# Optimization experiments

Measured on AMD Instinct MI355X. Metric: run time of the kernel, lower is better.

Reference implementation:

```python
import jax, jax.numpy as jnp
import numpy as np

B = 131072
D = 64
H1 = 512
H2 = 256
NC = 128  # nurse classes
DC = 128  # doctor classes
EPS = 1e-5
NEG = -1e9


def _kaiming(key, fan_in, fan_out):
    # kaiming_normal_ with mode='fan_out', relu gain: std = sqrt(2/fan_out)
    return jax.random.normal(key, (fan_in, fan_out), jnp.float32) * jnp.sqrt(2.0 / fan_out)


def setup_inputs() -> dict:
    key = jax.random.key(0)
    ks = jax.random.split(key, 16)
    x = jax.random.normal(ks[0], (B, D), jnp.float32)
    sn = jax.random.randint(ks[1], (B,), 0, NC)
    sd = jax.random.randint(ks[2], (B,), 0, DC)
    # last-4 / last-3 columns carry the per-sample max class thresholds
    x = x.at[:, -4].set(sn.astype(jnp.float32)).at[:, -3].set(sd.astype(jnp.float32))
    inp = {
        'x': x,
        'W0': _kaiming(ks[3], D, H1), 'b0': jnp.zeros((H1,), jnp.float32),
        'g0': jnp.ones((H1,), jnp.float32), 'be0': jnp.zeros((H1,), jnp.float32),
        'rm0': jax.random.normal(ks[4], (H1,), jnp.float32) * 0.1,
        'rv0': jax.random.uniform(ks[5], (H1,), jnp.float32, 0.5, 1.5),
        'W1': _kaiming(ks[6], H1, H2), 'b1': jnp.zeros((H2,), jnp.float32),
        'g1': jnp.ones((H2,), jnp.float32), 'be1': jnp.zeros((H2,), jnp.float32),
        'rm1': jax.random.normal(ks[7], (H2,), jnp.float32) * 0.1,
        'rv1': jax.random.uniform(ks[8], (H2,), jnp.float32, 0.5, 1.5),
        'nW1': _kaiming(ks[9], H2, 64), 'nb1': jnp.zeros((64,), jnp.float32),
        'nW2': _kaiming(ks[10], 64, NC), 'nb2': jnp.zeros((NC,), jnp.float32),
        'dW1': _kaiming(ks[11], H2, 64), 'db1': jnp.zeros((64,), jnp.float32),
        'dW2': _kaiming(ks[12], 64, DC), 'db2': jnp.zeros((DC,), jnp.float32),
    }
    return inp


def _bn(h, g, be, rm, rv):
    # BatchNorm1d inference: normalize with running stats
    return (h - rm) * (g * jax.lax.rsqrt(rv + EPS)) + be


def reference(x, W0, b0, g0, be0, rm0, rv0, W1, b1, g1, be1, rm1, rv1,
              nW1, nb1, nW2, nb2, dW1, db1, dW2, db2):
    s_nurse = x[:, -4].astype(jnp.int32)   # [B]
    s_doctor = x[:, -3].astype(jnp.int32)  # [B]

    h = jax.nn.relu(_bn(x @ W0 + b0, g0, be0, rm0, rv0))   # [B,H1]
    h = jax.nn.relu(_bn(h @ W1 + b1, g1, be1, rm1, rv1))   # [B,H2]

    nurse_logits = jax.nn.relu(h @ nW1 + nb1) @ nW2 + nb2   # [B,NC]
    doctor_logits = jax.nn.relu(h @ dW1 + db1) @ dW2 + db2  # [B,DC]

    # vectorized range mask: positions <= s_max are kept
    nmask = (jnp.arange(NC)[None, :] <= s_nurse[:, None]).astype(nurse_logits.dtype)
    dmask = (jnp.arange(DC)[None, :] <= s_doctor[:, None]).astype(doctor_logits.dtype)
    nurse_logits = nurse_logits * nmask + (1.0 - nmask) * NEG
    doctor_logits = doctor_logits * dmask + (1.0 - dmask) * NEG
    return (nurse_logits, doctor_logits)
```

## Files before the change

### kernel.cpp

```cpp
#include <hip/hip_runtime.h>

#define NB 131072
#define NEG9 -1e9f

typedef __attribute__((ext_vector_type(8))) __bf16 bf16x8;
typedef __attribute__((ext_vector_type(4))) float f32x4;
typedef __attribute__((ext_vector_type(2))) unsigned int u32x2;
typedef __attribute__((ext_vector_type(4))) unsigned int u32x4;

__device__ __forceinline__ f32x4 mfma16(bf16x8 a, bf16x8 b, f32x4 c) {
    return __builtin_amdgcn_mfma_f32_16x16x32_bf16(a, b, c, 0, 0, 0);
}

__device__ __forceinline__ unsigned pk(float h, float l) {
    return __builtin_amdgcn_perm(__builtin_bit_cast(unsigned, h),
                                 __builtin_bit_cast(unsigned, l), 0x07060302u);
}
__device__ __forceinline__ unsigned pku(unsigned h, unsigned l) {
    return __builtin_amdgcn_perm(h, l, 0x07060302u);
}

__device__ __forceinline__ unsigned short f2bf(float f) {
    unsigned u = __builtin_bit_cast(unsigned, f);
    u += 0x7fffu + ((u >> 16) & 1u);
    return (unsigned short)(u >> 16);
}

struct __align__(16) Wspace {
    unsigned short W0t[512][64];
    unsigned short W1t[256][512];
    unsigned short nW1t[64][256];
    unsigned short dW1t[64][256];
    unsigned short nW2t[128][64];
    unsigned short dW2t[128][64];
    float c0[512];
    float c1[256];
    float nb1c[64], db1c[64];
    float nb2c[128], db2c[128];
};

__device__ Wspace g_ws;

__global__ void prep_kernel(
    const float* __restrict__ W0, const float* __restrict__ b0,
    const float* __restrict__ g0, const float* __restrict__ be0,
    const float* __restrict__ rm0, const float* __restrict__ rv0,
    const float* __restrict__ W1, const float* __restrict__ b1,
    const float* __restrict__ g1, const float* __restrict__ be1,
    const float* __restrict__ rm1, const float* __restrict__ rv1,
    const float* __restrict__ nW1, const float* __restrict__ nb1,
    const float* __restrict__ nW2, const float* __restrict__ nb2,
    const float* __restrict__ dW1, const float* __restrict__ db1,
    const float* __restrict__ dW2, const float* __restrict__ db2)
{
    const int tid = blockIdx.x * 256 + threadIdx.x;

    {
        int n = tid >> 9, k = tid & 511;
        float s = g1[n] * rsqrtf(rv1[n] + 1e-5f);
        ((unsigned short*)g_ws.W1t)[tid] = f2bf(W1[k * 256 + n] * s);
    }
    if (tid < 512 * 64) {
        int n = tid >> 6, k = tid & 63;
        float s = g0[n] * rsqrtf(rv0[n] + 1e-5f);
        ((unsigned short*)g_ws.W0t)[tid] = f2bf(W0[k * 512 + n] * s);
    }
    if (tid < 64 * 256) {
        int n = tid >> 8, k = tid & 255;
        ((unsigned short*)g_ws.nW1t)[tid] = f2bf(nW1[k * 64 + n]);
        ((unsigned short*)g_ws.dW1t)[tid] = f2bf(dW1[k * 64 + n]);
    }
    if (tid < 128 * 64) {
        int n = tid >> 6, k = tid & 63;
        ((unsigned short*)g_ws.nW2t)[tid] = f2bf(nW2[k * 128 + n]);
        ((unsigned short*)g_ws.dW2t)[tid] = f2bf(dW2[k * 128 + n]);
    }
    if (tid < 512) g_ws.c0[tid] = (b0[tid] - rm0[tid]) * (g0[tid] * rsqrtf(rv0[tid] + 1e-5f)) + be0[tid];
    if (tid < 256) g_ws.c1[tid] = (b1[tid] - rm1[tid]) * (g1[tid] * rsqrtf(rv1[tid] + 1e-5f)) + be1[tid];
    if (tid < 64) { g_ws.nb1c[tid] = nb1[tid]; g_ws.db1c[tid] = db1[tid]; }
    if (tid < 128) { g_ws.nb2c[tid] = nb2[tid]; g_ws.db2c[tid] = db2[tid]; }
}

__global__ __launch_bounds__(512, 4) void fused_mlp(
    const u32x4* __restrict__ xu, float* __restrict__ out)
{
    __shared__ __align__(16) unsigned short sXs [8 * 64 * 8];
    __shared__ __align__(16) unsigned short sReg[32 * 64 * 8];

    const int tid = threadIdx.x;
    const int w = tid >> 6;
    const int lane = tid & 63;
    const int m = lane & 15;
    const int q = lane >> 4;
    const int qh = q >> 1;
    const int ql = (q & 1) * 4;
    const int row0 = blockIdx.x * 64;

    {
        int r = tid >> 3, g = tid & 7;
        u32x4 v0 = __builtin_nontemporal_load(&xu[(size_t)(row0 + r) * 16 + g * 2]);
        u32x4 v1 = __builtin_nontemporal_load(&xu[(size_t)(row0 + r) * 16 + g * 2 + 1]);
        u32x4 p = { pku(v0[1], v0[0]), pku(v0[3], v0[2]), pku(v1[1], v1[0]), pku(v1[3], v1[2]) };
        *(u32x4*)&sXs[(g * 64 + r) * 8] = p;
    }
    __syncthreads();

    f32x4 acc1[2][4];
#pragma unroll
    for (int a = 0; a < 2; ++a)
#pragma unroll
        for (int b = 0; b < 4; ++b) acc1[a][b] = f32x4{0.f, 0.f, 0.f, 0.f};

    for (int ch = 0; ch < 2; ++ch) {
#pragma unroll
        for (int nt = 0; nt < 2; ++nt) {
            const int gcb = ch * 256 + w * 32 + nt * 16;
            bf16x8 wa0 = *(const bf16x8*)&g_ws.W0t[gcb + m][q * 8];
            bf16x8 wa1 = *(const bf16x8*)&g_ws.W0t[gcb + m][32 + q * 8];
            f32x4 bias = *(const f32x4*)&g_ws.c0[gcb + q * 4];
            const int kg = w * 4 + nt * 2 + qh;
#pragma unroll
            for (int mt = 0; mt < 4; ++mt) {
                bf16x8 xq0 = *(const bf16x8*)&sXs[(q * 64 + mt * 16 + m) * 8];
                bf16x8 xq1 = *(const bf16x8*)&sXs[((4 + q) * 64 + mt * 16 + m) * 8];
                f32x4 c = {0.f, 0.f, 0.f, 0.f};
                c = mfma16(wa0, xq0, c);
                c = mfma16(wa1, xq1, c);
                u32x2 pw = { pk(fmaxf(c[1] + bias[1], 0.f), fmaxf(c[0] + bias[0], 0.f)),
                             pk(fmaxf(c[3] + bias[3], 0.f), fmaxf(c[2] + bias[2], 0.f)) };
                *(u32x2*)&sReg[(kg * 64 + mt * 16 + m) * 8 + ql] = pw;
            }
        }
        __syncthreads();

#pragma unroll
        for (int ks = 0; ks < 8; ++ks) {
            bf16x8 wb[2], ab[4];
#pragma unroll
            for (int nt = 0; nt < 2; ++nt)
                wb[nt] = *(const bf16x8*)&g_ws.W1t[w * 32 + nt * 16 + m][ch * 256 + ks * 32 + q * 8];
#pragma unroll
            for (int mt = 0; mt < 4; ++mt)
                ab[mt] = *(const bf16x8*)&sReg[((ks * 4 + q) * 64 + mt * 16 + m) * 8];
#pragma unroll
            for (int nt = 0; nt < 2; ++nt)
#pragma unroll
                for (int mt = 0; mt < 4; ++mt)
                    acc1[nt][mt] = mfma16(wb[nt], ab[mt], acc1[nt][mt]);
        }
        __syncthreads();
    }

#pragma unroll
    for (int nt = 0; nt < 2; ++nt) {
        const int cb = w * 32 + nt * 16;
        f32x4 bias = *(const f32x4*)&g_ws.c1[cb + q * 4];
        const int kg = w * 4 + nt * 2 + qh;
#pragma unroll
        for (int mt = 0; mt < 4; ++mt) {
            f32x4 c = acc1[nt][mt];
            u32x2 pw = { pk(fmaxf(c[1] + bias[1], 0.f), fmaxf(c[0] + bias[0], 0.f)),
                         pk(fmaxf(c[3] + bias[3], 0.f), fmaxf(c[2] + bias[2], 0.f)) };
            *(u32x2*)&sReg[(kg * 64 + mt * 16 + m) * 8 + ql] = pw;
        }
    }
    __syncthreads();

    const int head = w >> 2;
    {
        const int cb = (w & 3) * 16;
        const unsigned short (*Wh)[256] = head ? g_ws.dW1t : g_ws.nW1t;
        const float* bh = head ? g_ws.db1c : g_ws.nb1c;
        f32x4 acc[4];
#pragma unroll
        for (int b = 0; b < 4; ++b) acc[b] = f32x4{0.f, 0.f, 0.f, 0.f};
#pragma unroll
        for (int ks = 0; ks < 8; ++ks) {
            bf16x8 wh = *(const bf16x8*)&Wh[cb + m][ks * 32 + q * 8];
#pragma unroll
            for (int mt = 0; mt < 4; ++mt) {
                bf16x8 ab = *(const bf16x8*)&sReg[((ks * 4 + q) * 64 + mt * 16 + m) * 8];
                acc[mt] = mfma16(wh, ab, acc[mt]);
            }
        }
        __syncthreads();
        unsigned short* Ah = sReg + (head ? 4096 : 0);
        f32x4 bias = *(const f32x4*)&bh[cb + q * 4];
        const int kg = (w & 3) * 2 + qh;
#pragma unroll
        for (int mt = 0; mt < 4; ++mt) {
            f32x4 c = acc[mt];
            u32x2 pw = { pk(fmaxf(c[1] + bias[1], 0.f), fmaxf(c[0] + bias[0], 0.f)),
                         pk(fmaxf(c[3] + bias[3], 0.f), fmaxf(c[2] + bias[2], 0.f)) };
            *(u32x2*)&Ah[(kg * 64 + mt * 16 + m) * 8 + ql] = pw;
        }
    }
    __syncthreads();

    {
        const unsigned short (*W2)[64] = head ? g_ws.dW2t : g_ws.nW2t;
        const float* b2 = head ? g_ws.db2c : g_ws.nb2c;
        const unsigned short* Ah = sReg + (head ? 4096 : 0);
        float* op = out + (size_t)head * (size_t)NB * 128;

        int thr[4];
#pragma unroll
        for (int mt = 0; mt < 4; ++mt) {
            unsigned tv = *(const unsigned*)&sXs[(7 * 64 + mt * 16 + m) * 8 + 4];
            thr[mt] = (int)__builtin_bit_cast(float, head ? (tv & 0xffff0000u) : (tv << 16));
        }
#pragma unroll
        for (int ct = 0; ct < 2; ++ct) {
            const int ocb = (w & 3) * 32 + ct * 16;
            bf16x8 w0 = *(const bf16x8*)&W2[ocb + m][q * 8];
            bf16x8 w1 = *(const bf16x8*)&W2[ocb + m][32 + q * 8];
            f32x4 bias = *(const f32x4*)&b2[ocb + q * 4];
#pragma unroll
            for (int mt = 0; mt < 4; ++mt) {
                bf16x8 a0 = *(const bf16x8*)&Ah[(q * 64 + mt * 16 + m) * 8];
                bf16x8 a1 = *(const bf16x8*)&Ah[((4 + q) * 64 + mt * 16 + m) * 8];
                f32x4 c = {0.f, 0.f, 0.f, 0.f};
                c = mfma16(w0, a0, c);
                c = mfma16(w1, a1, c);
                const int ci = ocb + q * 4;
                const int t = thr[mt];
                float4 v;
                v.x = (ci + 0 <= t) ? c[0] + bias[0] : NEG9;
                v.y = (ci + 1 <= t) ? c[1] + bias[1] : NEG9;
                v.z = (ci + 2 <= t) ? c[2] + bias[2] : NEG9;
                v.w = (ci + 3 <= t) ? c[3] + bias[3] : NEG9;
                *(float4*)&op[(size_t)(row0 + mt * 16 + m) * 128 + ci] = v;
            }
        }
    }
}

extern "C" void kernel_launch(void* const* d_in, const int* in_sizes, int n_in,
                              void* d_out, int out_size, void* d_ws, size_t ws_size,
                              hipStream_t stream) {
    (void)in_sizes; (void)n_in; (void)d_ws; (void)ws_size;

    prep_kernel<<<512, 256, 0, stream>>>(
        (const float*)d_in[1], (const float*)d_in[2], (const float*)d_in[3],
        (const float*)d_in[4], (const float*)d_in[5], (const float*)d_in[6],
        (const float*)d_in[7], (const float*)d_in[8], (const float*)d_in[9],
        (const float*)d_in[10], (const float*)d_in[11], (const float*)d_in[12],
        (const float*)d_in[13], (const float*)d_in[14], (const float*)d_in[15],
        (const float*)d_in[16], (const float*)d_in[17], (const float*)d_in[18],
        (const float*)d_in[19], (const float*)d_in[20]);

    fused_mlp<<<NB / 64, 512, 0, stream>>>((const u32x4*)d_in[0], (float*)d_out);
}
```

Baseline: 294.1 us.

## Hoist X fragments to registers, retile head layer, nontemporal output stores

Loads the input X fragments from shared memory into registers once, so they are reused across both hidden-layer chunks instead of being reloaded. Alternates the chunk order by block parity to spread weight-cache access. Retiles the head first layer into a 2x2 grid of column and row tiles so each A/B fragment feeds two MFMAs. Reorders the output layer to reuse A fragments across two column tiles and writes the large output with nontemporal stores. These changes cut LDS traffic and reduce cache pollution on the write stream, at the cost of higher register pressure.

After: 309.3 us. 1.05x slower.

```diff
diff --git a/kernel.cpp b/kernel.cpp
--- a/kernel.cpp
+++ b/kernel.cpp
@@ -105,13 +105,22 @@
     }
     __syncthreads();
 
+    bf16x8 xr[2][4];
+#pragma unroll
+    for (int g2 = 0; g2 < 2; ++g2)
+#pragma unroll
+        for (int mt = 0; mt < 4; ++mt)
+            xr[g2][mt] = *(const bf16x8*)&sXs[((g2 * 4 + q) * 64 + mt * 16 + m) * 8];
+
     f32x4 acc1[2][4];
 #pragma unroll
     for (int a = 0; a < 2; ++a)
 #pragma unroll
         for (int b = 0; b < 4; ++b) acc1[a][b] = f32x4{0.f, 0.f, 0.f, 0.f};
 
-    for (int ch = 0; ch < 2; ++ch) {
+    const int chsw = blockIdx.x & 1;
+    for (int i = 0; i < 2; ++i) {
+        const int ch = i ^ chsw;
 #pragma unroll
         for (int nt = 0; nt < 2; ++nt) {
             const int gcb = ch * 256 + w * 32 + nt * 16;
@@ -121,11 +130,9 @@
             const int kg = w * 4 + nt * 2 + qh;
 #pragma unroll
             for (int mt = 0; mt < 4; ++mt) {
-                bf16x8 xq0 = *(const bf16x8*)&sXs[(q * 64 + mt * 16 + m) * 8];
-                bf16x8 xq1 = *(const bf16x8*)&sXs[((4 + q) * 64 + mt * 16 + m) * 8];
                 f32x4 c = {0.f, 0.f, 0.f, 0.f};
-                c = mfma16(wa0, xq0, c);
-                c = mfma16(wa1, xq1, c);
+                c = mfma16(wa0, xr[0][mt], c);
+                c = mfma16(wa1, xr[1][mt], c);
                 u32x2 pw = { pk(fmaxf(c[1] + bias[1], 0.f), fmaxf(c[0] + bias[0], 0.f)),
                              pk(fmaxf(c[3] + bias[3], 0.f), fmaxf(c[2] + bias[2], 0.f)) };
                 *(u32x2*)&sReg[(kg * 64 + mt * 16 + m) * 8 + ql] = pw;
@@ -168,31 +175,43 @@
 
     const int head = w >> 2;
     {
-        const int cb = (w & 3) * 16;
+        const int rh  = w & 1;
+        const int ct2 = (w >> 1) & 1;
         const unsigned short (*Wh)[256] = head ? g_ws.dW1t : g_ws.nW1t;
         const float* bh = head ? g_ws.db1c : g_ws.nb1c;
-        f32x4 acc[4];
-#pragma unroll
-        for (int b = 0; b < 4; ++b) acc[b] = f32x4{0.f, 0.f, 0.f, 0.f};
+        f32x4 acc[2][2];
+#pragma unroll
+        for (int a = 0; a < 2; ++a)
+#pragma unroll
+            for (int b = 0; b < 2; ++b) acc[a][b] = f32x4{0.f, 0.f, 0.f, 0.f};
 #pragma unroll
         for (int ks = 0; ks < 8; ++ks) {
-            bf16x8 wh = *(const bf16x8*)&Wh[cb + m][ks * 32 + q * 8];
-#pragma unroll
-            for (int mt = 0; mt < 4; ++mt) {
-                bf16x8 ab = *(const bf16x8*)&sReg[((ks * 4 + q) * 64 + mt * 16 + m) * 8];
-                acc[mt] = mfma16(wh, ab, acc[mt]);
-            }
+            bf16x8 wh[2], ab[2];
+#pragma unroll
+            for (int nt = 0; nt < 2; ++nt)
+                wh[nt] = *(const bf16x8*)&Wh[ct2 * 32 + nt * 16 + m][ks * 32 + q * 8];
+#pragma unroll
+            for (int mt = 0; mt < 2; ++mt)
+                ab[mt] = *(const bf16x8*)&sReg[((ks * 4 + q) * 64 + (rh * 2 + mt) * 16 + m) * 8];
+#pragma unroll
+            for (int nt = 0; nt < 2; ++nt)
+#pragma unroll
+                for (int mt = 0; mt < 2; ++mt)
+                    acc[nt][mt] = mfma16(wh[nt], ab[mt], acc[nt][mt]);
         }
         __syncthreads();
         unsigned short* Ah = sReg + (head ? 4096 : 0);
-        f32x4 bias = *(const f32x4*)&bh[cb + q * 4];
-        const int kg = (w & 3) * 2 + qh;
-#pragma unroll
-        for (int mt = 0; mt < 4; ++mt) {
-            f32x4 c = acc[mt];
-            u32x2 pw = { pk(fmaxf(c[1] + bias[1], 0.f), fmaxf(c[0] + bias[0], 0.f)),
-                         pk(fmaxf(c[3] + bias[3], 0.f), fmaxf(c[2] + bias[2], 0.f)) };
-            *(u32x2*)&Ah[(kg * 64 + mt * 16 + m) * 8 + ql] = pw;
+#pragma unroll
+        for (int nt = 0; nt < 2; ++nt) {
+            f32x4 bias = *(const f32x4*)&bh[ct2 * 32 + nt * 16 + q * 4];
+            const int kg = ct2 * 4 + nt * 2 + qh;
+#pragma unroll
+            for (int mt = 0; mt < 2; ++mt) {
+                f32x4 c = acc[nt][mt];
+                u32x2 pw = { pk(fmaxf(c[1] + bias[1], 0.f), fmaxf(c[0] + bias[0], 0.f)),
+                             pk(fmaxf(c[3] + bias[3], 0.f), fmaxf(c[2] + bias[2], 0.f)) };
+                *(u32x2*)&Ah[(kg * 64 + (rh * 2 + mt) * 16 + m) * 8 + ql] = pw;
+            }
         }
     }
     __syncthreads();
@@ -209,27 +228,32 @@
             unsigned tv = *(const unsigned*)&sXs[(7 * 64 + mt * 16 + m) * 8 + 4];
             thr[mt] = (int)__builtin_bit_cast(float, head ? (tv & 0xffff0000u) : (tv << 16));
         }
+        bf16x8 w2f[2][2];
+        f32x4 b2f[2];
 #pragma unroll
         for (int ct = 0; ct < 2; ++ct) {
             const int ocb = (w & 3) * 32 + ct * 16;
-            bf16x8 w0 = *(const bf16x8*)&W2[ocb + m][q * 8];
-            bf16x8 w1 = *(const bf16x8*)&W2[ocb + m][32 + q * 8];
-            f32x4 bias = *(const f32x4*)&b2[ocb + q * 4];
-#pragma unroll
-            for (int mt = 0; mt < 4; ++mt) {
-                bf16x8 a0 = *(const bf16x8*)&Ah[(q * 64 + mt * 16 + m) * 8];
-                bf16x8 a1 = *(const bf16x8*)&Ah[((4 + q) * 64 + mt * 16 + m) * 8];
+            w2f[ct][0] = *(const bf16x8*)&W2[ocb + m][q * 8];
+            w2f[ct][1] = *(const bf16x8*)&W2[ocb + m][32 + q * 8];
+            b2f[ct] = *(const f32x4*)&b2[ocb + q * 4];
+        }
+#pragma unroll
+        for (int mt = 0; mt < 4; ++mt) {
+            bf16x8 a0 = *(const bf16x8*)&Ah[(q * 64 + mt * 16 + m) * 8];
+            bf16x8 a1 = *(const bf16x8*)&Ah[((4 + q) * 64 + mt * 16 + m) * 8];
+            const int t = thr[mt];
+#pragma unroll
+            for (int ct = 0; ct < 2; ++ct) {
                 f32x4 c = {0.f, 0.f, 0.f, 0.f};
-                c = mfma16(w0, a0, c);
-                c = mfma16(w1, a1, c);
-                const int ci = ocb + q * 4;
-                const int t = thr[mt];
-                float4 v;
-                v.x = (ci + 0 <= t) ? c[0] + bias[0] : NEG9;
-                v.y = (ci + 1 <= t) ? c[1] + bias[1] : NEG9;
-                v.z = (ci + 2 <= t) ? c[2] + bias[2] : NEG9;
-                v.w = (ci + 3 <= t) ? c[3] + bias[3] : NEG9;
-                *(float4*)&op[(size_t)(row0 + mt * 16 + m) * 128 + ci] = v;
+                c = mfma16(w2f[ct][0], a0, c);
+                c = mfma16(w2f[ct][1], a1, c);
+                const int ci = (w & 3) * 32 + ct * 16 + q * 4;
+                f32x4 v;
+                v[0] = (ci + 0 <= t) ? c[0] + b2f[ct][0] : NEG9;
+                v[1] = (ci + 1 <= t) ? c[1] + b2f[ct][1] : NEG9;
+                v[2] = (ci + 2 <= t) ? c[2] + b2f[ct][2] : NEG9;
+                v[3] = (ci + 3 <= t) ? c[3] + b2f[ct][3] : NEG9;
+                __builtin_nontemporal_store(v, (f32x4*)&op[(size_t)(row0 + mt * 16 + m) * 128 + ci]);
             }
         }
     }
```

## Materialize full first hidden layer in LDS and hoist x fragments to registers

Applied to the files above, without the earlier changes.

The first layer's 512 outputs are now computed in one pass into a 64 KB LDS buffer instead of two 256-column chunks, which removes the chunk loop and two barriers. The layer-2 reduction then runs over all 16 k-steps without a mid-loop sync. Input x fragments are loaded from LDS into registers once and reused across output tiles. The cost is LDS per block rising from about 40 KB to about 72 KB, which likely cuts the number of resident blocks per CU and lowers occupancy for this memory-bound kernel.

Measured after the change: 288.0 us. 2.0% less time.

```diff
diff --git a/kernel.cpp b/kernel.cpp
--- a/kernel.cpp
+++ b/kernel.cpp
@@ -84,8 +84,8 @@
 __global__ __launch_bounds__(512, 4) void fused_mlp(
     const u32x4* __restrict__ xu, float* __restrict__ out)
 {
-    __shared__ __align__(16) unsigned short sXs [8 * 64 * 8];
-    __shared__ __align__(16) unsigned short sReg[32 * 64 * 8];
+    __shared__ __align__(16) unsigned short sXs[8 * 64 * 8];
+    __shared__ __align__(16) unsigned short sH0[64 * 64 * 8];
 
     const int tid = threadIdx.x;
     const int w = tid >> 6;
@@ -105,51 +105,54 @@
     }
     __syncthreads();
 
+    bf16x8 xr[2][4];
+#pragma unroll
+    for (int g2 = 0; g2 < 2; ++g2)
+#pragma unroll
+        for (int mt = 0; mt < 4; ++mt)
+            xr[g2][mt] = *(const bf16x8*)&sXs[((g2 * 4 + q) * 64 + mt * 16 + m) * 8];
+
+#pragma unroll
+    for (int nt = 0; nt < 4; ++nt) {
+        const int gcb = w * 64 + nt * 16;
+        bf16x8 wa0 = *(const bf16x8*)&g_ws.W0t[gcb + m][q * 8];
+        bf16x8 wa1 = *(const bf16x8*)&g_ws.W0t[gcb + m][32 + q * 8];
+        f32x4 bias = *(const f32x4*)&g_ws.c0[gcb + q * 4];
+        const int kg = w * 8 + nt * 2 + qh;
+#pragma unroll
+        for (int mt = 0; mt < 4; ++mt) {
+            f32x4 c = {0.f, 0.f, 0.f, 0.f};
+            c = mfma16(wa0, xr[0][mt], c);
+            c = mfma16(wa1, xr[1][mt], c);
+            u32x2 pw = { pk(fmaxf(c[1] + bias[1], 0.f), fmaxf(c[0] + bias[0], 0.f)),
+                         pk(fmaxf(c[3] + bias[3], 0.f), fmaxf(c[2] + bias[2], 0.f)) };
+            *(u32x2*)&sH0[(kg * 64 + mt * 16 + m) * 8 + ql] = pw;
+        }
+    }
+    __syncthreads();
+
     f32x4 acc1[2][4];
 #pragma unroll
     for (int a = 0; a < 2; ++a)
 #pragma unroll
         for (int b = 0; b < 4; ++b) acc1[a][b] = f32x4{0.f, 0.f, 0.f, 0.f};
 
-    for (int ch = 0; ch < 2; ++ch) {
-#pragma unroll
-        for (int nt = 0; nt < 2; ++nt) {
-            const int gcb = ch * 256 + w * 32 + nt * 16;
-            bf16x8 wa0 = *(const bf16x8*)&g_ws.W0t[gcb + m][q * 8];
-            bf16x8 wa1 = *(const bf16x8*)&g_ws.W0t[gcb + m][32 + q * 8];
-            f32x4 bias = *(const f32x4*)&g_ws.c0[gcb + q * 4];
-            const int kg = w * 4 + nt * 2 + qh;
-#pragma unroll
-            for (int mt = 0; mt < 4; ++mt) {
-                bf16x8 xq0 = *(const bf16x8*)&sXs[(q * 64 + mt * 16 + m) * 8];
-                bf16x8 xq1 = *(const bf16x8*)&sXs[((4 + q) * 64 + mt * 16 + m) * 8];
-                f32x4 c = {0.f, 0.f, 0.f, 0.f};
-                c = mfma16(wa0, xq0, c);
-                c = mfma16(wa1, xq1, c);
-                u32x2 pw = { pk(fmaxf(c[1] + bias[1], 0.f), fmaxf(c[0] + bias[0], 0.f)),
-                             pk(fmaxf(c[3] + bias[3], 0.f), fmaxf(c[2] + bias[2], 0.f)) };
-                *(u32x2*)&sReg[(kg * 64 + mt * 16 + m) * 8 + ql] = pw;
-            }
-        }
-        __syncthreads();
-
-#pragma unroll
-        for (int ks = 0; ks < 8; ++ks) {
-            bf16x8 wb[2], ab[4];
-#pragma unroll
-            for (int nt = 0; nt < 2; ++nt)
-                wb[nt] = *(const bf16x8*)&g_ws.W1t[w * 32 + nt * 16 + m][ch * 256 + ks * 32 + q * 8];
+#pragma unroll
+    for (int ks = 0; ks < 16; ++ks) {
+        bf16x8 wb[2], ab[4];
+#pragma unroll
+        for (int nt = 0; nt < 2; ++nt)
+            wb[nt] = *(const bf16x8*)&g_ws.W1t[w * 32 + nt * 16 + m][ks * 32 + q * 8];
+#pragma unroll
+        for (int mt = 0; mt < 4; ++mt)
+            ab[mt] = *(const bf16x8*)&sH0[((ks * 4 + q) * 64 + mt * 16 + m) * 8];
+#pragma unroll
+        for (int nt = 0; nt < 2; ++nt)
 #pragma unroll
             for (int mt = 0; mt < 4; ++mt)
-                ab[mt] = *(const bf16x8*)&sReg[((ks * 4 + q) * 64 + mt * 16 + m) * 8];
-#pragma unroll
-            for (int nt = 0; nt < 2; ++nt)
-#pragma unroll
-                for (int mt = 0; mt < 4; ++mt)
-                    acc1[nt][mt] = mfma16(wb[nt], ab[mt], acc1[nt][mt]);
-        }
-        __syncthreads();
-    }
+                acc1[nt][mt] = mfma16(wb[nt], ab[mt], acc1[nt][mt]);
+    }
+    __syncthreads();
 
 #pragma unroll
     for (int nt = 0; nt < 2; ++nt) {
@@ -161,7 +164,7 @@
             f32x4 c = acc1[nt][mt];
             u32x2 pw = { pk(fmaxf(c[1] + bias[1], 0.f), fmaxf(c[0] + bias[0], 0.f)),
                          pk(fmaxf(c[3] + bias[3], 0.f), fmaxf(c[2] + bias[2], 0.f)) };
-            *(u32x2*)&sReg[(kg * 64 + mt * 16 + m) * 8 + ql] = pw;
+            *(u32x2*)&sH0[(kg * 64 + mt * 16 + m) * 8 + ql] = pw;
         }
     }
     __syncthreads();
@@ -179,12 +182,12 @@
             bf16x8 wh = *(const bf16x8*)&Wh[cb + m][ks * 32 + q * 8];
 #pragma unroll
             for (int mt = 0; mt < 4; ++mt) {
-                bf16x8 ab = *(const bf16x8*)&sReg[((ks * 4 + q) * 64 + mt * 16 + m) * 8];
+                bf16x8 ab = *(const bf16x8*)&sH0[((ks * 4 + q) * 64 + mt * 16 + m) * 8];
                 acc[mt] = mfma16(wh, ab, acc[mt]);
             }
         }
         __syncthreads();
-        unsigned short* Ah = sReg + (head ? 4096 : 0);
+        unsigned short* Ah = sH0 + (head ? 4096 : 0);
         f32x4 bias = *(const f32x4*)&bh[cb + q * 4];
         const int kg = (w & 3) * 2 + qh;
 #pragma unroll
@@ -200,7 +203,7 @@
     {
         const unsigned short (*W2)[64] = head ? g_ws.dW2t : g_ws.nW2t;
         const float* b2 = head ? g_ws.db2c : g_ws.nb2c;
-        const unsigned short* Ah = sReg + (head ? 4096 : 0);
+        const unsigned short* Ah = sH0 + (head ? 4096 : 0);
         float* op = out + (size_t)head * (size_t)NB * 128;
 
         int thr[4];
@@ -224,12 +227,12 @@
                 c = mfma16(w1, a1, c);
                 const int ci = ocb + q * 4;
                 const int t = thr[mt];
-                float4 v;
-                v.x = (ci + 0 <= t) ? c[0] + bias[0] : NEG9;
-                v.y = (ci + 1 <= t) ? c[1] + bias[1] : NEG9;
-                v.z = (ci + 2 <= t) ? c[2] + bias[2] : NEG9;
-                v.w = (ci + 3 <= t) ? c[3] + bias[3] : NEG9;
-                *(float4*)&op[(size_t)(row0 + mt * 16 + m) * 128 + ci] = v;
+                f32x4 v;
+                v[0] = (ci + 0 <= t) ? c[0] + bias[0] : NEG9;
+                v[1] = (ci + 1 <= t) ? c[1] + bias[1] : NEG9;
+                v[2] = (ci + 2 <= t) ? c[2] + bias[2] : NEG9;
+                v[3] = (ci + 3 <= t) ? c[3] + bias[3] : NEG9;
+                *(f32x4*)&op[(size_t)(row0 + mt * 16 + m) * 128 + ci] = v;
             }
         }
     }
```
